# Performance work log

Measured on AMD Instinct MI355X. Metric: run time of the kernel, lower is better.

## Reference

```python
import jax, jax.numpy as jnp
import numpy as np

ANCHORS = np.array([[10.0, 13.0], [16.0, 30.0], [33.0, 23.0]], dtype=np.float32)
NUM_ANCHORS = 3
NUM_CLASSES = 80
OBJ_SCALE = 1.0
NOOBJ_SCALE = 100.0
EPS = 1e-12


def setup_inputs() -> dict:
    key = jax.random.key(0)
    ks = jax.random.split(key, 10)
    B, A, G, C = 32, NUM_ANCHORS, 52, NUM_CLASSES
    x = jax.random.normal(ks[0], (B, A * (C + 5), G, G), dtype=jnp.float32)
    tx = jax.random.uniform(ks[1], (B, A, G, G), dtype=jnp.float32)
    ty = jax.random.uniform(ks[2], (B, A, G, G), dtype=jnp.float32)
    tw = jax.random.normal(ks[3], (B, A, G, G), dtype=jnp.float32)
    th = jax.random.normal(ks[4], (B, A, G, G), dtype=jnp.float32)
    tconf = jax.random.uniform(ks[5], (B, A, G, G), dtype=jnp.float32)
    tcls = jax.random.uniform(ks[6], (B, A, G, G, C), dtype=jnp.float32)
    sum_weights1 = jax.random.uniform(ks[7], (B, A, G, G), dtype=jnp.float32)
    obj_mask = jax.random.randint(ks[8], (B, A, G, G), 0, 2).astype(bool)
    noobj_mask = jax.random.randint(ks[9], (B, A, G, G), 0, 2).astype(bool)
    return {"x": x, "tx": tx, "ty": ty, "tw": tw, "th": th, "tconf": tconf,
            "tcls": tcls, "sum_weights1": sum_weights1, "obj_mask": obj_mask,
            "noobj_mask": noobj_mask, "img_dim": 416}


def _bce(p, t):
    # torch BCELoss(reduction='none') on already-sigmoided probs
    return -(t * jnp.log(jnp.clip(p, EPS, 1.0)) + (1.0 - t) * jnp.log(jnp.clip(1.0 - p, EPS, 1.0)))


def reference(x, tx, ty, tw, th, tconf, tcls, sum_weights1, obj_mask, noobj_mask, img_dim):
    B, _, G, _ = x.shape
    A, C = NUM_ANCHORS, NUM_CLASSES
    stride = img_dim / G  # python float
    # [B, A, G, G, C+5]
    pred = x.reshape(B, A, C + 5, G, G).transpose(0, 1, 3, 4, 2)
    px = jax.nn.sigmoid(pred[..., 0])
    py = jax.nn.sigmoid(pred[..., 1])
    pw = pred[..., 2]
    ph = pred[..., 3]
    pred_conf = jax.nn.sigmoid(pred[..., 4])
    pred_cls = jax.nn.sigmoid(pred[..., 5:])

    grid_x = jnp.arange(G, dtype=x.dtype).reshape(1, 1, 1, G)  # varies along last axis
    grid_y = jnp.arange(G, dtype=x.dtype).reshape(1, 1, G, 1)
    scaled_anchors = jnp.asarray(ANCHORS) / jnp.asarray(stride, x.dtype)
    anchor_w = scaled_anchors[:, 0].reshape(1, A, 1, 1)
    anchor_h = scaled_anchors[:, 1].reshape(1, A, 1, 1)

    sg = jax.lax.stop_gradient  # mimics .data in pred_boxes construction
    pred_boxes = jnp.stack([
        sg(px) + jnp.broadcast_to(grid_x, px.shape),
        sg(py) + jnp.broadcast_to(grid_y, py.shape),
        jnp.exp(sg(pw)) * jnp.broadcast_to(anchor_w, pw.shape),
        jnp.exp(sg(ph)) * jnp.broadcast_to(anchor_h, ph.shape),
    ], axis=-1)  # [B, A, G, G, 4]

    output = jnp.concatenate([
        pred_boxes.reshape(B, -1, 4) * stride,
        pred_conf.reshape(B, -1, 1),
        pred_cls.reshape(B, -1, C),
    ], axis=-1)

    om = obj_mask.astype(x.dtype)
    nm = noobj_mask.astype(x.dtype)
    n_obj = jnp.maximum(om.sum(), 1.0)
    n_noobj = jnp.maximum(nm.sum(), 1.0)

    def wmse(p, t):
        # mean over obj elements of mse * sum_weights1
        return jnp.sum(om * (p - t) ** 2 * sum_weights1) / n_obj

    loss_x = wmse(px, tx)
    loss_y = wmse(py, ty)
    loss_w = wmse(pw, tw)
    loss_h = wmse(ph, th)

    bce_conf = _bce(pred_conf, tconf)
    loss_conf_obj = jnp.sum(om * bce_conf * sum_weights1) / n_obj
    loss_conf_noobj = jnp.sum(nm * bce_conf) / n_noobj
    loss_conf = OBJ_SCALE * loss_conf_obj + NOOBJ_SCALE * loss_conf_noobj

    # tcls[obj_mask] yields [N, C]; mean is over N*C
    loss_cls = jnp.sum(om[..., None] * _bce(pred_cls, tcls)) / (n_obj * C)

    total_loss = loss_x + loss_y + loss_w + loss_h + loss_conf + loss_cls
    return output, total_loss
```

## Files before the change

kernel.cpp:

```cpp
#include <hip/hip_runtime.h>

#define NB 32
#define NA 3
#define GD 52
#define GG 2704
#define NC 80
#define CHN 85
#define CPW 16
#define WPP 169
#define NPLANE (NB * NA)
#define NWAVE (NPLANE * WPP)
#define WPB 4
#define NBLK (NWAVE / WPB)
#define NXQ 340
#define LXW 1360
#define AUXW 160

__device__ __forceinline__ float sigm_u(float u) { return __builtin_amdgcn_rcpf(u); }

__global__ __launch_bounds__(256) void yolo_main(
    const float* __restrict__ x,
    const float* __restrict__ tx, const float* __restrict__ ty,
    const float* __restrict__ tw, const float* __restrict__ th,
    const float* __restrict__ tconf, const float* __restrict__ tcls,
    const float* __restrict__ sw1,
    const int* __restrict__ om, const int* __restrict__ nm,
    const int* __restrict__ imgdim,
    float* __restrict__ out,
    float4* __restrict__ partials,
    double* __restrict__ accD)
{
    __shared__ float lx_all[WPB * LXW];
    __shared__ float la_all[WPB * AUXW];

    const int tid  = threadIdx.x;
    const int widx = tid >> 6, lane = tid & 63;
    const int wid  = blockIdx.x * WPB + widx;
    const int plane = wid / WPP;
    const int sblk  = wid - plane * WPP;
    const int a = plane % NA, b = plane / NA;
    const int s0 = sblk * CPW;
    float* lx = lx_all + widx * LXW;
    float* la = la_all + widx * AUXW;

    int iv = imgdim[0];
    float imgf = (iv > 0 && iv < 65536) ? (float)iv : __int_as_float(iv);
    const float stride = imgf / (float)GD;
    const float aw = (a == 0) ? 10.0f : ((a == 1) ? 16.0f : 33.0f);
    const float ah = (a == 0) ? 13.0f : ((a == 1) ? 30.0f : 23.0f);

    const long pbase = (long)plane * GG + s0;
    const float* xb = x + ((long)b * (NA * CHN) + a * CHN) * GG + s0;
    const float* tb = tcls + pbase * NC;

    float v0 = 0.0f, v1 = 0.0f;
    if (lane < CPW) {
        float vtx = tx[pbase + lane],    vty = ty[pbase + lane];
        float vtw = tw[pbase + lane],    vth = th[pbase + lane];
        float vtc = tconf[pbase + lane], vsw = sw1[pbase + lane];
        float vom = (float)om[pbase + lane], vnm = (float)nm[pbase + lane];
        int gcell = s0 + lane;
        int gyi = gcell / GD;
        la[0 * CPW + lane] = vtx;  la[1 * CPW + lane] = vty;
        la[2 * CPW + lane] = vtw;  la[3 * CPW + lane] = vth;
        la[4 * CPW + lane] = vtc;  la[5 * CPW + lane] = vom * vsw;
        la[6 * CPW + lane] = vnm;  la[7 * CPW + lane] = vom;
        la[8 * CPW + lane] = (float)(gcell - gyi * GD);
        la[9 * CPW + lane] = (float)gyi;
        v0 = vom; v1 = vnm;
    }

    float4 xr[6];
    #pragma unroll
    for (int k = 0; k < 6; ++k) {
        int q = lane + 64 * k;
        if (q < NXQ) {
            int ch = q >> 2, sq = (q & 3) << 2;
            xr[k] = *(const float4*)(xb + (long)ch * GG + sq);
        }
    }
    __builtin_amdgcn_wave_barrier();

    float4 tr[5]; float gk[5];
    #pragma unroll
    for (int k = 0; k < 5; ++k) {
        int q = lane + 64 * k;
        int s = q / 20, c4 = (q - s * 20) * 4;
        float g = la[7 * CPW + s];
        gk[k] = g;
        if (g != 0.0f) tr[k] = *(const float4*)(tb + s * NC + c4);
    }

    float s_obj = 0.f, s_cn = 0.f, s_cl = 0.f;

    #pragma unroll
    for (int k = 0; k < 6; ++k) {
        int q = lane + 64 * k;
        if (q >= NXQ) continue;
        int ch = q >> 2, sq = (q & 3) << 2;
        float vv[4] = { xr[k].x, xr[k].y, xr[k].z, xr[k].w };
        if (ch >= 5) {
            #pragma unroll
            for (int j = 0; j < 4; ++j)
                lx[(sq + j) * CHN + ch] = sigm_u(1.0f + __expf(-vv[j]));
        } else if (ch == 0) {
            #pragma unroll
            for (int j = 0; j < 4; ++j) {
                int s = sq + j;
                float p = sigm_u(1.0f + __expf(-vv[j]));
                float d = p - la[0 * CPW + s];
                s_obj = fmaf(la[5 * CPW + s], d * d, s_obj);
                lx[s * CHN + 0] = (p + la[8 * CPW + s]) * stride;
            }
        } else if (ch == 1) {
            #pragma unroll
            for (int j = 0; j < 4; ++j) {
                int s = sq + j;
                float p = sigm_u(1.0f + __expf(-vv[j]));
                float d = p - la[1 * CPW + s];
                s_obj = fmaf(la[5 * CPW + s], d * d, s_obj);
                lx[s * CHN + 1] = (p + la[9 * CPW + s]) * stride;
            }
        } else if (ch == 2) {
            #pragma unroll
            for (int j = 0; j < 4; ++j) {
                int s = sq + j;
                float d = vv[j] - la[2 * CPW + s];
                s_obj = fmaf(la[5 * CPW + s], d * d, s_obj);
                lx[s * CHN + 2] = __expf(vv[j]) * aw;
            }
        } else if (ch == 3) {
            #pragma unroll
            for (int j = 0; j < 4; ++j) {
                int s = sq + j;
                float d = vv[j] - la[3 * CPW + s];
                s_obj = fmaf(la[5 * CPW + s], d * d, s_obj);
                lx[s * CHN + 3] = __expf(vv[j]) * ah;
            }
        } else {
            #pragma unroll
            for (int j = 0; j < 4; ++j) {
                int s = sq + j;
                float z = vv[j];
                float u = 1.0f + __expf(-z);
                float p = sigm_u(u);
                float t = la[4 * CPW + s];
                float bb = fmaf(1.0f - t, z, __logf(u));
                s_obj = fmaf(la[5 * CPW + s], bb, s_obj);
                s_cn  = fmaf(la[6 * CPW + s], bb, s_cn);
                lx[s * CHN + 4] = p;
            }
        }
    }
    __builtin_amdgcn_wave_barrier();

    float* ob = out + pbase * CHN;
    #pragma unroll
    for (int k = 0; k < 6; ++k) {
        int q = lane + 64 * k;
        if (q < NXQ) {
            float4 w4 = *(const float4*)&lx[4 * q];
            *(float4*)(ob + 4 * q) = w4;
        }
    }

    #pragma unroll
    for (int k = 0; k < 5; ++k) {
        if (gk[k] != 0.0f) {
            int q = lane + 64 * k;
            int s = q / 20, c4 = (q - s * 20) * 4;
            int base = s * CHN + 5 + c4;
            float tt[4] = { tr[k].x, tr[k].y, tr[k].z, tr[k].w };
            #pragma unroll
            for (int j = 0; j < 4; ++j) {
                float p = lx[base + j];
                s_cl -= fmaf(tt[j], __logf(p), (1.0f - tt[j]) * __logf(1.0f - p));
            }
        }
    }
    s_obj = fmaf(s_cl, 0.0125f, s_obj);

    float v2 = s_obj, v3 = s_cn;
    #pragma unroll
    for (int off = 32; off > 0; off >>= 1) {
        v0 += __shfl_down(v0, off, 64);
        v1 += __shfl_down(v1, off, 64);
        v2 += __shfl_down(v2, off, 64);
        v3 += __shfl_down(v3, off, 64);
    }
    if (lane == 0) {
        if (partials) {
            partials[wid] = make_float4(v0, v1, v2, v3);
        } else {
            atomicAdd(&accD[0], (double)v0);
            atomicAdd(&accD[8], (double)v1);
            atomicAdd(&accD[16], (double)v2);
            atomicAdd(&accD[24], (double)v3);
        }
    }
}

__global__ __launch_bounds__(256) void yolo_reduce(const float4* __restrict__ partials,
                                                   float* __restrict__ out_loss)
{
    __shared__ double sred[4][4];
    const int tid = threadIdx.x, wv = tid >> 6, ln = tid & 63;
    double d0 = 0, d1 = 0, d2 = 0, d3 = 0;
    for (int i = tid; i < NWAVE; i += 256) {
        float4 p = partials[i];
        d0 += (double)p.x; d1 += (double)p.y; d2 += (double)p.z; d3 += (double)p.w;
    }
    #pragma unroll
    for (int off = 32; off > 0; off >>= 1) {
        d0 += __shfl_down(d0, off, 64);
        d1 += __shfl_down(d1, off, 64);
        d2 += __shfl_down(d2, off, 64);
        d3 += __shfl_down(d3, off, 64);
    }
    if (ln == 0) { sred[wv][0] = d0; sred[wv][1] = d1; sred[wv][2] = d2; sred[wv][3] = d3; }
    __syncthreads();
    if (tid == 0) {
        double t0 = sred[0][0] + sred[1][0] + sred[2][0] + sred[3][0];
        double t1 = sred[0][1] + sred[1][1] + sred[2][1] + sred[3][1];
        double t2 = sred[0][2] + sred[1][2] + sred[2][2] + sred[3][2];
        double t3 = sred[0][3] + sred[1][3] + sred[2][3] + sred[3][3];
        double nobj = fmax(t0, 1.0), nnoobj = fmax(t1, 1.0);
        *out_loss = (float)(t2 / nobj + 100.0 * t3 / nnoobj);
    }
}

__global__ void yolo_final_atomic(const double* __restrict__ accD, float* __restrict__ out_loss)
{
    double nobj = fmax(accD[0], 1.0), nnoobj = fmax(accD[8], 1.0);
    *out_loss = (float)(accD[16] / nobj + 100.0 * accD[24] / nnoobj);
}

extern "C" void kernel_launch(void* const* d_in, const int* in_sizes, int n_in,
                              void* d_out, int out_size, void* d_ws, size_t ws_size,
                              hipStream_t stream)
{
    const float* x     = (const float*)d_in[0];
    const float* tx    = (const float*)d_in[1];
    const float* ty    = (const float*)d_in[2];
    const float* tw    = (const float*)d_in[3];
    const float* th    = (const float*)d_in[4];
    const float* tconf = (const float*)d_in[5];
    const float* tcls  = (const float*)d_in[6];
    const float* sw1   = (const float*)d_in[7];
    const int*   om    = (const int*)d_in[8];
    const int*   nm    = (const int*)d_in[9];
    const int*   img   = (const int*)d_in[10];
    float* out = (float*)d_out;

    const size_t need = (size_t)NWAVE * sizeof(float4);
    dim3 grid(NBLK);

    if (ws_size >= need) {
        float4* partials = (float4*)d_ws;
        yolo_main<<<grid, 256, 0, stream>>>(x, tx, ty, tw, th, tconf, tcls, sw1,
                                            om, nm, img, out, partials, nullptr);
        yolo_reduce<<<1, 256, 0, stream>>>(partials, out + (out_size - 1));
    } else {
        double* accD = (double*)d_ws;
        hipMemsetAsync(d_ws, 0, 32 * sizeof(double), stream);
        yolo_main<<<grid, 256, 0, stream>>>(x, tx, ty, tw, th, tconf, tcls, sw1,
                                            om, nm, img, out, nullptr, accD);
        yolo_final_atomic<<<1, 1, 0, stream>>>(accD, out + (out_size - 1));
    }
}
```

Baseline: 66.51 us.

## Halve cells per wave and split loss reduction into two-stage multi-block pass

Each wave now handles 8 grid cells instead of 16, doubling the number of waves and halving per-wave register and LDS footprint, which should raise occupancy. The single-block double-precision reduction of per-wave partials becomes a 32-block float reduction followed by a tiny final kernel, so the larger partials array is summed in parallel. This adds an extra kernel launch, more partial writes, and float rather than double accumulation in the first stage, which may change rounding slightly.

```diff
diff --git a/kernel.cpp b/kernel.cpp
--- a/kernel.cpp
+++ b/kernel.cpp
@@ -6,15 +6,17 @@
 #define GG 2704
 #define NC 80
 #define CHN 85
-#define CPW 16
-#define WPP 169
+#define CPW 8
+#define WPP 338
 #define NPLANE (NB * NA)
 #define NWAVE (NPLANE * WPP)
 #define WPB 4
 #define NBLK (NWAVE / WPB)
-#define NXQ 340
-#define LXW 1360
-#define AUXW 160
+#define NXQ 170
+#define NTQ 160
+#define LXW 680
+#define AUXW 80
+#define RBLK 32
 
 __device__ __forceinline__ float sigm_u(float u) { return __builtin_amdgcn_rcpf(u); }
 
@@ -70,34 +72,37 @@
         v0 = vom; v1 = vnm;
     }
 
-    float4 xr[6];
-    #pragma unroll
-    for (int k = 0; k < 6; ++k) {
+    float4 xr[3];
+    #pragma unroll
+    for (int k = 0; k < 3; ++k) {
         int q = lane + 64 * k;
         if (q < NXQ) {
-            int ch = q >> 2, sq = (q & 3) << 2;
+            int ch = q >> 1, sq = (q & 1) << 2;
             xr[k] = *(const float4*)(xb + (long)ch * GG + sq);
         }
     }
     __builtin_amdgcn_wave_barrier();
 
-    float4 tr[5]; float gk[5];
-    #pragma unroll
-    for (int k = 0; k < 5; ++k) {
-        int q = lane + 64 * k;
-        int s = q / 20, c4 = (q - s * 20) * 4;
-        float g = la[7 * CPW + s];
-        gk[k] = g;
-        if (g != 0.0f) tr[k] = *(const float4*)(tb + s * NC + c4);
+    float4 tr[3]; float gk[3];
+    #pragma unroll
+    for (int k = 0; k < 3; ++k) {
+        gk[k] = 0.0f;
+        int q = lane + 64 * k;
+        if (q < NTQ) {
+            int s = q / 20, c4 = (q - s * 20) * 4;
+            float g = la[7 * CPW + s];
+            gk[k] = g;
+            if (g != 0.0f) tr[k] = *(const float4*)(tb + s * NC + c4);
+        }
     }
 
     float s_obj = 0.f, s_cn = 0.f, s_cl = 0.f;
 
     #pragma unroll
-    for (int k = 0; k < 6; ++k) {
+    for (int k = 0; k < 3; ++k) {
         int q = lane + 64 * k;
         if (q >= NXQ) continue;
-        int ch = q >> 2, sq = (q & 3) << 2;
+        int ch = q >> 1, sq = (q & 1) << 2;
         float vv[4] = { xr[k].x, xr[k].y, xr[k].z, xr[k].w };
         if (ch >= 5) {
             #pragma unroll
@@ -156,7 +161,7 @@
 
     float* ob = out + pbase * CHN;
     #pragma unroll
-    for (int k = 0; k < 6; ++k) {
+    for (int k = 0; k < 3; ++k) {
         int q = lane + 64 * k;
         if (q < NXQ) {
             float4 w4 = *(const float4*)&lx[4 * q];
@@ -165,7 +170,7 @@
     }
 
     #pragma unroll
-    for (int k = 0; k < 5; ++k) {
+    for (int k = 0; k < 3; ++k) {
         if (gk[k] != 0.0f) {
             int q = lane + 64 * k;
             int s = q / 20, c4 = (q - s * 20) * 4;
@@ -200,15 +205,15 @@
     }
 }
 
-__global__ __launch_bounds__(256) void yolo_reduce(const float4* __restrict__ partials,
-                                                   float* __restrict__ out_loss)
-{
-    __shared__ double sred[4][4];
+__global__ __launch_bounds__(256) void yolo_reduceA(const float4* __restrict__ partials,
+                                                    float4* __restrict__ stage2)
+{
+    __shared__ float sred[4][4];
     const int tid = threadIdx.x, wv = tid >> 6, ln = tid & 63;
-    double d0 = 0, d1 = 0, d2 = 0, d3 = 0;
-    for (int i = tid; i < NWAVE; i += 256) {
+    float d0 = 0, d1 = 0, d2 = 0, d3 = 0;
+    for (int i = blockIdx.x * 256 + tid; i < NWAVE; i += RBLK * 256) {
         float4 p = partials[i];
-        d0 += (double)p.x; d1 += (double)p.y; d2 += (double)p.z; d3 += (double)p.w;
+        d0 += p.x; d1 += p.y; d2 += p.z; d3 += p.w;
     }
     #pragma unroll
     for (int off = 32; off > 0; off >>= 1) {
@@ -219,13 +224,32 @@
     }
     if (ln == 0) { sred[wv][0] = d0; sred[wv][1] = d1; sred[wv][2] = d2; sred[wv][3] = d3; }
     __syncthreads();
-    if (tid == 0) {
-        double t0 = sred[0][0] + sred[1][0] + sred[2][0] + sred[3][0];
-        double t1 = sred[0][1] + sred[1][1] + sred[2][1] + sred[3][1];
-        double t2 = sred[0][2] + sred[1][2] + sred[2][2] + sred[3][2];
-        double t3 = sred[0][3] + sred[1][3] + sred[2][3] + sred[3][3];
-        double nobj = fmax(t0, 1.0), nnoobj = fmax(t1, 1.0);
-        *out_loss = (float)(t2 / nobj + 100.0 * t3 / nnoobj);
+    if (tid == 0)
+        stage2[blockIdx.x] = make_float4(sred[0][0] + sred[1][0] + sred[2][0] + sred[3][0],
+                                         sred[0][1] + sred[1][1] + sred[2][1] + sred[3][1],
+                                         sred[0][2] + sred[1][2] + sred[2][2] + sred[3][2],
+                                         sred[0][3] + sred[1][3] + sred[2][3] + sred[3][3]);
+}
+
+__global__ __launch_bounds__(64) void yolo_reduceB(const float4* __restrict__ stage2,
+                                                   float* __restrict__ out_loss)
+{
+    const int ln = threadIdx.x;
+    double d0 = 0, d1 = 0, d2 = 0, d3 = 0;
+    if (ln < RBLK) {
+        float4 p = stage2[ln];
+        d0 = p.x; d1 = p.y; d2 = p.z; d3 = p.w;
+    }
+    #pragma unroll
+    for (int off = 32; off > 0; off >>= 1) {
+        d0 += __shfl_down(d0, off, 64);
+        d1 += __shfl_down(d1, off, 64);
+        d2 += __shfl_down(d2, off, 64);
+        d3 += __shfl_down(d3, off, 64);
+    }
+    if (ln == 0) {
+        double nobj = fmax(d0, 1.0), nnoobj = fmax(d1, 1.0);
+        *out_loss = (float)(d2 / nobj + 100.0 * d3 / nnoobj);
     }
 }
 
@@ -252,14 +276,16 @@
     const int*   img   = (const int*)d_in[10];
     float* out = (float*)d_out;
 
-    const size_t need = (size_t)NWAVE * sizeof(float4);
+    const size_t need = (size_t)(NWAVE + RBLK) * sizeof(float4);
     dim3 grid(NBLK);
 
     if (ws_size >= need) {
         float4* partials = (float4*)d_ws;
+        float4* stage2   = partials + NWAVE;
         yolo_main<<<grid, 256, 0, stream>>>(x, tx, ty, tw, th, tconf, tcls, sw1,
                                             om, nm, img, out, partials, nullptr);
-        yolo_reduce<<<1, 256, 0, stream>>>(partials, out + (out_size - 1));
+        yolo_reduceA<<<RBLK, 256, 0, stream>>>(partials, stage2);
+        yolo_reduceB<<<1, 64, 0, stream>>>(stage2, out + (out_size - 1));
     } else {
         double* accD = (double*)d_ws;
         hipMemsetAsync(d_ws, 0, 32 * sizeof(double), stream);
```

Result: faster. 57.67 us (-13.3%).
